# Kernel optimization log

Hardware: AMD Instinct MI355X
Metric: run time of the kernel (lower is better)

The kernel has to match this reference:

```python
import jax, jax.numpy as jnp
import numpy as np

B, T, D = 8, 2048, 512
F = 512          # filters (== D due to residual add)
K = 7            # kernel_size
H = 128          # hidden_dim of kernel generator (hard-coded in source)
LN_EPS = 1e-3    # keras LayerNormalization default epsilon


def setup_inputs() -> dict:
    key = jax.random.key(0)
    ks = jax.random.split(key, 8)
    x = jax.random.normal(ks[0], (B, T, D), dtype=jnp.float32)
    # kernel generator: Dense(D->H, relu) then Dense(H->K*F)
    W1 = jax.random.normal(ks[1], (D, H), dtype=jnp.float32) * (1.0 / np.sqrt(D))
    b1 = jnp.zeros((H,), dtype=jnp.float32)
    W2 = jax.random.normal(ks[2], (H, K * F), dtype=jnp.float32) * (1.0 / np.sqrt(H))
    b2 = jnp.zeros((K * F,), dtype=jnp.float32)
    # LayerNorm params
    gamma = jnp.ones((F,), dtype=jnp.float32)
    beta = jnp.zeros((F,), dtype=jnp.float32)
    return {"x": x, "W1": W1, "b1": b1, "W2": W2, "b2": b2,
            "gamma": gamma, "beta": beta}


def _dynamic_conv_block(x, W1, b1, W2, b2, gamma, beta):
    # per-token dynamic kernels: [B, T, K, F]
    h = jax.nn.relu(jnp.einsum("btd,dh->bth", x, W1) + b1)
    kernels = (jnp.einsum("bth,hf->btf", h, W2) + b2).reshape(B, T, K, F)
    # extract sliding-window patches (same padding): [B, T, K, D]
    pad = K // 2
    xp = jnp.pad(x, ((0, 0), (pad, pad), (0, 0)))
    patches = jnp.stack([xp[:, i:i + T, :] for i in range(K)], axis=2)
    # per-token conv: contract over window K and input channels D
    conv_out = jnp.einsum("btkd,btkf->btf", patches, kernels)
    # residual + LayerNorm + relu (dropout is identity at inference)
    y = conv_out + x
    mu = jnp.mean(y, axis=-1, keepdims=True)
    var = jnp.mean(jnp.square(y - mu), axis=-1, keepdims=True)
    y = (y - mu) * jax.lax.rsqrt(var + LN_EPS) * gamma + beta
    return jax.nn.relu(y)


def reference(x, W1, b1, W2, b2, gamma, beta):
    return _dynamic_conv_block(x, W1, b1, W2, b2, gamma, beta)
```

## Files before the change

### kernel.cpp

```cpp
#include <hip/hip_runtime.h>

#define NT 2048
#define ND 512
#define NH 128
#define NKW 7
#define NTOK 16384

typedef float f32x4 __attribute__((ext_vector_type(4)));
typedef __bf16 bf16x8 __attribute__((ext_vector_type(8)));
typedef unsigned short u16;
typedef unsigned int u32;
typedef u16 u16x8 __attribute__((ext_vector_type(8)));

__device__ __forceinline__ u16 f2bf(float f){
  u32 u = __builtin_bit_cast(u32, f);
  return (u16)((u + 0x7fffu + ((u>>16)&1u)) >> 16);
}
__device__ __forceinline__ float bf2f(u16 s){
  u32 u = ((u32)s)<<16;
  return __builtin_bit_cast(float, u);
}
__device__ __forceinline__ bf16x8 pack8(const float4& a, const float4& b){
  u16x8 u;
  u[0]=f2bf(a.x); u[1]=f2bf(a.y); u[2]=f2bf(a.z); u[3]=f2bf(a.w);
  u[4]=f2bf(b.x); u[5]=f2bf(b.y); u[6]=f2bf(b.z); u[7]=f2bf(b.w);
  return __builtin_bit_cast(bf16x8, u);
}
__device__ __forceinline__ void store16(void* p, const u16 u[8]){
  u32 d0 = (u32)u[0] | ((u32)u[1]<<16);
  u32 d1 = (u32)u[2] | ((u32)u[3]<<16);
  u32 d2 = (u32)u[4] | ((u32)u[5]<<16);
  u32 d3 = (u32)u[6] | ((u32)u[7]<<16);
  int4 vv; vv.x=(int)d0; vv.y=(int)d1; vv.z=(int)d2; vv.w=(int)d3;
  *(int4*)p = vv;
}

__global__ __launch_bounds__(256) void prep2_kernel(
    const float* __restrict__ W1, const float* __restrict__ W2,
    const float* __restrict__ b2, u16* __restrict__ W1F, u16* __restrict__ B3)
{
  int f = blockIdx.x*256 + threadIdx.x;
  u16 u[8];
  if (f < 8192){
    int n = f & 127, sk = f >> 7, kb = sk*8;
    #pragma unroll
    for (int j=0;j<8;++j) u[j] = f2bf(W1[(size_t)(kb+j)*NH + n]);
    store16(W1F + (size_t)f*8, u);
  } else {
    int g = f - 8192;
    int n = g & 511, sc = g >> 9, kb = sc*8;
    if (kb < 896){
      int kwin = kb >> 7, h = kb & 127;
      #pragma unroll
      for (int j=0;j<8;++j) u[j] = f2bf(W2[(size_t)(h+j)*(NKW*ND) + kwin*ND + n]);
    } else {
      int jb = kb - 896;
      #pragma unroll
      for (int j=0;j<8;++j){ int jj = jb+j; u[j] = (jj<NKW)? f2bf(b2[(size_t)jj*ND + n]) : (u16)0; }
    }
    store16(B3 + (size_t)g*8, u);
  }
}

__global__ __launch_bounds__(512,2) void fused_kernel(
    const float* __restrict__ x, const u16* __restrict__ W1F,
    const float* __restrict__ b1, const u16* __restrict__ B3,
    const float* __restrict__ gamma, const float* __restrict__ beta,
    float* __restrict__ out)
{
  __shared__ __align__(16) u16 h_lds[2*64*64];
  __shared__ __align__(16) u16 At0[64*64], At1[64*64];
  __shared__ float rs_lds[70];
  __shared__ float s_lds[64][8];
  __shared__ float red_s[64][8], red_q[64][8];
  __shared__ float mu_lds[64], rstd_lds[64];

  const int tid = threadIdx.x, w = tid>>6, l = tid&63;
  const int m_base = blockIdx.x*64;

  #pragma unroll
  for (int r=0;r<8;++r){
    int row = w*8 + r;
    const float4* pr = (const float4*)(x + (size_t)(m_base+row)*ND + l*8);
    float4 a = pr[0], b = pr[1];
    float s = (a.x+a.y)+(a.z+a.w)+((b.x+b.y)+(b.z+b.w));
    s += __shfl_xor(s,1); s += __shfl_xor(s,2); s += __shfl_xor(s,4);
    s += __shfl_xor(s,8); s += __shfl_xor(s,16); s += __shfl_xor(s,32);
    if (l==0) rs_lds[3+row] = s;
  }
  if (w < 6){
    int j = (w<3)? w : w+64;
    int tg2 = m_base + j - 3;
    float s2 = 0.f;
    if (tg2 >= 0 && tg2 < NTOK){
      const float4* p2 = (const float4*)(x + (size_t)tg2*ND + l*8);
      float4 a = p2[0], b = p2[1];
      s2 = (a.x+a.y)+(a.z+a.w)+((b.x+b.y)+(b.z+b.w));
    }
    s2 += __shfl_xor(s2,1); s2 += __shfl_xor(s2,2); s2 += __shfl_xor(s2,4);
    s2 += __shfl_xor(s2,8); s2 += __shfl_xor(s2,16); s2 += __shfl_xor(s2,32);
    if (l==0) rs_lds[j] = s2;
  }
  __syncthreads();
  {
    int rr = tid>>3, k = tid&7;
    float v = 0.f;
    if (k < NKW){
      int ti = (m_base+rr) & (NT-1);
      int idx = ti + k - 3;
      if (idx >= 0 && idx < NT) v = rs_lds[rr+k];
    }
    s_lds[rr][k] = v;
  }

  {
    const int wm = w>>2, wn = w&3;
    f32x4 acc1[2][2] = {};
    #pragma unroll
    for (int kc=0;kc<16;++kc){
      bf16x8 af[2], bfr[2];
      #pragma unroll
      for (int mi=0;mi<2;++mi){
        int row = wm*32 + mi*16 + (l&15);
        const float4* px = (const float4*)(x + (size_t)(m_base+row)*ND + kc*32 + (l>>4)*8);
        af[mi] = pack8(px[0], px[1]);
      }
      #pragma unroll
      for (int ni=0;ni<2;++ni){
        int n = wn*32 + ni*16 + (l&15);
        bfr[ni] = *(const bf16x8*)(W1F + ((size_t)(kc*4 + (l>>4))*128 + n)*8);
      }
      #pragma unroll
      for (int mi=0;mi<2;++mi)
        #pragma unroll
        for (int ni=0;ni<2;++ni)
          acc1[mi][ni] = __builtin_amdgcn_mfma_f32_16x16x32_bf16(af[mi], bfr[ni], acc1[mi][ni],0,0,0);
    }
    #pragma unroll
    for (int ni=0;ni<2;++ni){
      int col = wn*32 + ni*16 + (l&15);
      float bias = b1[col];
      int half = col>>6, cc = col&63;
      #pragma unroll
      for (int mi=0;mi<2;++mi)
        #pragma unroll
        for (int r=0;r<4;++r){
          int row = wm*32 + mi*16 + (l>>4)*4 + r;
          float v = fmaxf(acc1[mi][ni][r] + bias, 0.f);
          int byte = half*8192 + row*128 + ((cc*2) ^ ((row&7)<<4));
          *(u16*)((char*)h_lds + byte) = f2bf(v);
        }
    }
  }
  __syncthreads();

  f32x4 acc[4][4] = {};
  bf16x8 bE[2][4], bO[2][4];
  const int row3 = tid>>3, slot = tid&7;

  auto loadB = [&](int c, bf16x8 (&bf)[2][4]){
    #pragma unroll
    for (int kk=0;kk<2;++kk)
      #pragma unroll
      for (int ni=0;ni<4;++ni){
        int rowB = w*64 + ni*16 + (l&15);
        bf[kk][ni] = *(const bf16x8*)(B3 + ((size_t)((c*2+kk)*4 + (l>>4))*512 + rowB)*8);
      }
  };
  auto stageA = [&](u16* dst, int c){
    u16 u[8];
    if (c < 14){
      float sv = s_lds[row3][c>>1];
      const char* src = (const char*)h_lds + (c&1)*8192 + row3*128 + ((slot*16) ^ ((row3&7)<<4));
      u16x8 hv = *(const u16x8*)src;
      #pragma unroll
      for (int j=0;j<8;++j) u[j] = f2bf(bf2f(hv[j])*sv);
    } else {
      #pragma unroll
      for (int j=0;j<8;++j){
        int e2 = slot*8+j;
        u[j] = (e2<NKW)? f2bf(s_lds[row3][e2]) : (u16)0;
      }
    }
    store16((char*)dst + row3*128 + ((slot*16) ^ ((row3&7)<<4)), u);
  };
  auto mfmaC = [&](const u16* A, bf16x8 (&b)[2][4]){
    __builtin_amdgcn_s_setprio(1);
    #pragma unroll
    for (int kk=0;kk<2;++kk){
      bf16x8 af[4];
      #pragma unroll
      for (int mi=0;mi<4;++mi){
        int r2 = mi*16 + (l&15);
        int byte = r2*128 + (((kk*64)+((l>>4)*16)) ^ ((r2&7)<<4));
        af[mi] = *(const bf16x8*)((const char*)A + byte);
      }
      #pragma unroll
      for (int mi=0;mi<4;++mi)
        #pragma unroll
        for (int ni=0;ni<4;++ni)
          acc[mi][ni] = __builtin_amdgcn_mfma_f32_16x16x32_bf16(af[mi], b[kk][ni], acc[mi][ni],0,0,0);
    }
    __builtin_amdgcn_s_setprio(0);
  };
  #define SYNC() do{ __builtin_amdgcn_sched_barrier(0); \
      asm volatile("s_waitcnt lgkmcnt(0)" ::: "memory"); \
      __builtin_amdgcn_s_barrier(); \
      __builtin_amdgcn_sched_barrier(0); }while(0)

  loadB(0, bE);
  stageA(At0, 0);
  SYNC();
  #pragma unroll
  for (int t=0;t<7;++t){
    loadB(2*t+1, bO);
    stageA(At1, 2*t+1);
    mfmaC(At0, bE);
    SYNC();
    loadB(2*t+2, bE);
    stageA(At0, 2*t+2);
    mfmaC(At1, bO);
    SYNC();
  }
  mfmaC(At0, bE);
  #undef SYNC

  #pragma unroll
  for (int mi=0;mi<4;++mi){
    #pragma unroll
    for (int r=0;r<4;++r){
      int m = mi*16 + (l>>4)*4 + r;
      int tg = m_base + m;
      float ps=0.f, pq=0.f;
      #pragma unroll
      for (int ni=0;ni<4;++ni){
        int n = w*64 + ni*16 + (l&15);
        float v = acc[mi][ni][r] + x[(size_t)tg*ND + n];
        acc[mi][ni][r] = v;
        ps += v; pq += v*v;
      }
      #pragma unroll
      for (int msk=1; msk<16; msk<<=1){ ps += __shfl_xor(ps,msk); pq += __shfl_xor(pq,msk); }
      if ((l&15)==0){ red_s[m][w]=ps; red_q[m][w]=pq; }
    }
  }
  __syncthreads();
  if (tid < 64){
    float ssum=0.f, sq=0.f;
    #pragma unroll
    for (int ww=0; ww<8; ++ww){ ssum += red_s[tid][ww]; sq += red_q[tid][ww]; }
    float mu = ssum * (1.0f/ND);
    float var = sq*(1.0f/ND) - mu*mu;
    mu_lds[tid] = mu;
    rstd_lds[tid] = rsqrtf(var + 1e-3f);
  }
  __syncthreads();
  float gv[4], bv[4];
  #pragma unroll
  for (int ni=0;ni<4;++ni){
    int n = w*64 + ni*16 + (l&15);
    gv[ni] = gamma[n]; bv[ni] = beta[n];
  }
  #pragma unroll
  for (int mi=0;mi<4;++mi){
    #pragma unroll
    for (int r=0;r<4;++r){
      int m = mi*16 + (l>>4)*4 + r;
      int tg = m_base + m;
      float mu = mu_lds[m], rstd = rstd_lds[m];
      #pragma unroll
      for (int ni=0;ni<4;++ni){
        int n = w*64 + ni*16 + (l&15);
        float v = (acc[mi][ni][r]-mu)*rstd*gv[ni] + bv[ni];
        out[(size_t)tg*ND + n] = fmaxf(v, 0.f);
      }
    }
  }
}

extern "C" void kernel_launch(void* const* d_in, const int* in_sizes, int n_in,
                              void* d_out, int out_size, void* d_ws, size_t ws_size,
                              hipStream_t stream)
{
  (void)in_sizes; (void)n_in; (void)out_size; (void)ws_size;
  const float* x     = (const float*)d_in[0];
  const float* W1    = (const float*)d_in[1];
  const float* b1    = (const float*)d_in[2];
  const float* W2    = (const float*)d_in[3];
  const float* b2    = (const float*)d_in[4];
  const float* gamma = (const float*)d_in[5];
  const float* beta  = (const float*)d_in[6];
  float* out = (float*)d_out;

  char* ws = (char*)d_ws;
  u16* W1F = (u16*)(ws);
  u16* B3  = (u16*)(ws + 131072);

  prep2_kernel<<<272, 256, 0, stream>>>(W1, W2, b2, W1F, B3);
  fused_kernel<<<256, 512, 0, stream>>>(x, W1F, b1, B3, gamma, beta, out);
}
```

Before: 139.6 us.

## Build MFMA A-fragments in registers from h_lds, dropping staged A buffers and barriers

Instead of staging a scaled A tile into double-buffered LDS (At0/At1) with block-wide barriers per chunk, each wave now reads h directly from h_lds, scales it by per-row s values preloaded into registers, and converts to bf16 in registers before the MFMAs. The bias chunk becomes a single MFMA using only the first k-slice. This removes the LDS writes, the extra reads and the 15 barriers in the main loop. In exchange every wave redoes the scaling and conversion for all 64 rows instead of sharing it, which adds VALU work and register pressure.

Result: no change. 140.2 us (+0.4%).

```diff
diff --git a/kernel.cpp b/kernel.cpp
--- a/kernel.cpp
+++ b/kernel.cpp
@@ -1,4 +1,5 @@
 #include <hip/hip_runtime.h>
+#include <utility>
 
 #define NT 2048
 #define ND 512
@@ -12,6 +13,8 @@
 typedef unsigned int u32;
 typedef u16 u16x8 __attribute__((ext_vector_type(8)));
 
+template<int N> using IC = std::integral_constant<int, N>;
+
 __device__ __forceinline__ u16 f2bf(float f){
   u32 u = __builtin_bit_cast(u32, f);
   return (u16)((u + 0x7fffu + ((u>>16)&1u)) >> 16);
@@ -25,14 +28,6 @@
   u[0]=f2bf(a.x); u[1]=f2bf(a.y); u[2]=f2bf(a.z); u[3]=f2bf(a.w);
   u[4]=f2bf(b.x); u[5]=f2bf(b.y); u[6]=f2bf(b.z); u[7]=f2bf(b.w);
   return __builtin_bit_cast(bf16x8, u);
-}
-__device__ __forceinline__ void store16(void* p, const u16 u[8]){
-  u32 d0 = (u32)u[0] | ((u32)u[1]<<16);
-  u32 d1 = (u32)u[2] | ((u32)u[3]<<16);
-  u32 d2 = (u32)u[4] | ((u32)u[5]<<16);
-  u32 d3 = (u32)u[6] | ((u32)u[7]<<16);
-  int4 vv; vv.x=(int)d0; vv.y=(int)d1; vv.z=(int)d2; vv.w=(int)d3;
-  *(int4*)p = vv;
 }
 
 __global__ __launch_bounds__(256) void prep2_kernel(
@@ -45,7 +40,10 @@
     int n = f & 127, sk = f >> 7, kb = sk*8;
     #pragma unroll
     for (int j=0;j<8;++j) u[j] = f2bf(W1[(size_t)(kb+j)*NH + n]);
-    store16(W1F + (size_t)f*8, u);
+    u16x8 v;
+    #pragma unroll
+    for (int j=0;j<8;++j) v[j]=u[j];
+    *(u16x8*)(W1F + (size_t)f*8) = v;
   } else {
     int g = f - 8192;
     int n = g & 511, sc = g >> 9, kb = sc*8;
@@ -58,7 +56,10 @@
       #pragma unroll
       for (int j=0;j<8;++j){ int jj = jb+j; u[j] = (jj<NKW)? f2bf(b2[(size_t)jj*ND + n]) : (u16)0; }
     }
-    store16(B3 + (size_t)g*8, u);
+    u16x8 v;
+    #pragma unroll
+    for (int j=0;j<8;++j) v[j]=u[j];
+    *(u16x8*)(B3 + (size_t)g*8) = v;
   }
 }
 
@@ -69,9 +70,8 @@
     float* __restrict__ out)
 {
   __shared__ __align__(16) u16 h_lds[2*64*64];
-  __shared__ __align__(16) u16 At0[64*64], At1[64*64];
   __shared__ float rs_lds[70];
-  __shared__ float s_lds[64][8];
+  __shared__ __align__(16) float s_lds[64][8];
   __shared__ float red_s[64][8], red_q[64][8];
   __shared__ float mu_lds[64], rstd_lds[64];
 
@@ -156,7 +156,16 @@
 
   f32x4 acc[4][4] = {};
   bf16x8 bE[2][4], bO[2][4];
-  const int row3 = tid>>3, slot = tid&7;
+
+  float sr[4][8];
+  #pragma unroll
+  for (int mi=0;mi<4;++mi){
+    int r = mi*16 + (l&15);
+    f32x4 a0 = *(const f32x4*)&s_lds[r][0];
+    f32x4 a1 = *(const f32x4*)&s_lds[r][4];
+    #pragma unroll
+    for (int j=0;j<4;++j){ sr[mi][j] = a0[j]; sr[mi][4+j] = a1[j]; }
+  }
 
   auto loadB = [&](int c, bf16x8 (&bf)[2][4]){
     #pragma unroll
@@ -167,63 +176,55 @@
         bf[kk][ni] = *(const bf16x8*)(B3 + ((size_t)((c*2+kk)*4 + (l>>4))*512 + rowB)*8);
       }
   };
-  auto stageA = [&](u16* dst, int c){
-    u16 u[8];
-    if (c < 14){
-      float sv = s_lds[row3][c>>1];
-      const char* src = (const char*)h_lds + (c&1)*8192 + row3*128 + ((slot*16) ^ ((row3&7)<<4));
-      u16x8 hv = *(const u16x8*)src;
-      #pragma unroll
-      for (int j=0;j<8;++j) u[j] = f2bf(bf2f(hv[j])*sv);
-    } else {
-      #pragma unroll
-      for (int j=0;j<8;++j){
-        int e2 = slot*8+j;
-        u[j] = (e2<NKW)? f2bf(s_lds[row3][e2]) : (u16)0;
-      }
-    }
-    store16((char*)dst + row3*128 + ((slot*16) ^ ((row3&7)<<4)), u);
-  };
-  auto mfmaC = [&](const u16* A, bf16x8 (&b)[2][4]){
-    __builtin_amdgcn_s_setprio(1);
+  auto chunk = [&](auto kcC, bf16x8 (&b)[2][4]){
+    constexpr int kc = decltype(kcC)::value;
     #pragma unroll
     for (int kk=0;kk<2;++kk){
       bf16x8 af[4];
       #pragma unroll
       for (int mi=0;mi<4;++mi){
-        int r2 = mi*16 + (l&15);
-        int byte = r2*128 + (((kk*64)+((l>>4)*16)) ^ ((r2&7)<<4));
-        af[mi] = *(const bf16x8*)((const char*)A + byte);
-      }
+        int r = mi*16 + (l&15);
+        const char* hp = (const char*)h_lds + (kc&1)*8192 + r*128
+                         + (((kk*64) + ((l>>4)*16)) ^ ((r&7)<<4));
+        u16x8 hv = *(const u16x8*)hp;
+        float sv = sr[mi][kc>>1];
+        #pragma unroll
+        for (int j=0;j<8;++j) af[mi][j] = (__bf16)(bf2f(hv[j]) * sv);
+      }
+      __builtin_amdgcn_s_setprio(1);
       #pragma unroll
       for (int mi=0;mi<4;++mi)
         #pragma unroll
         for (int ni=0;ni<4;++ni)
           acc[mi][ni] = __builtin_amdgcn_mfma_f32_16x16x32_bf16(af[mi], b[kk][ni], acc[mi][ni],0,0,0);
-    }
-    __builtin_amdgcn_s_setprio(0);
+      __builtin_amdgcn_s_setprio(0);
+    }
   };
-  #define SYNC() do{ __builtin_amdgcn_sched_barrier(0); \
-      asm volatile("s_waitcnt lgkmcnt(0)" ::: "memory"); \
-      __builtin_amdgcn_s_barrier(); \
-      __builtin_amdgcn_sched_barrier(0); }while(0)
+  #define SB0 __builtin_amdgcn_sched_barrier(0)
 
   loadB(0, bE);
-  stageA(At0, 0);
-  SYNC();
-  #pragma unroll
-  for (int t=0;t<7;++t){
-    loadB(2*t+1, bO);
-    stageA(At1, 2*t+1);
-    mfmaC(At0, bE);
-    SYNC();
-    loadB(2*t+2, bE);
-    stageA(At0, 2*t+2);
-    mfmaC(At1, bO);
-    SYNC();
-  }
-  mfmaC(At0, bE);
-  #undef SYNC
+  SB0;
+  #define PAIR(T) \
+    loadB(2*(T)+1, bO); SB0; chunk(IC<2*(T)>{}, bE); \
+    loadB(2*(T)+2, bE); SB0; chunk(IC<2*(T)+1>{}, bO);
+  PAIR(0) PAIR(1) PAIR(2) PAIR(3) PAIR(4) PAIR(5) PAIR(6)
+  #undef PAIR
+  {
+    bf16x8 af[4];
+    const bool g0 = ((l>>4)==0);
+    #pragma unroll
+    for (int mi=0;mi<4;++mi){
+      #pragma unroll
+      for (int j=0;j<7;++j) af[mi][j] = g0 ? (__bf16)sr[mi][j] : (__bf16)0.f;
+      af[mi][7] = (__bf16)0.f;
+    }
+    #pragma unroll
+    for (int mi=0;mi<4;++mi)
+      #pragma unroll
+      for (int ni=0;ni<4;++ni)
+        acc[mi][ni] = __builtin_amdgcn_mfma_f32_16x16x32_bf16(af[mi], bE[0][ni], acc[mi][ni],0,0,0);
+  }
+  #undef SB0
 
   #pragma unroll
   for (int mi=0;mi<4;++mi){
```
